# Kernel optimization log

Hardware: AMD Instinct MI355X
Metric: run time of the kernel (lower is better)

## Reference

```python
import math
import jax, jax.numpy as jnp
import numpy as np
from jax.scipy.linalg import solve_triangular

K, D, Q = 512, 2048, 8
B = 8192
EPS = 1e-5
RHO0 = math.log(math.exp(1.0) - 1.0)  # softplus^-1(1.0), matches psi_init=scale_init=1.0


def setup_inputs() -> dict:
    key = jax.random.key(0)
    k1, k2, k3, k4, k5 = jax.random.split(key, 5)
    x = jax.random.normal(k1, (B, D), dtype=jnp.float32)
    mu = jax.random.normal(k2, (K, D), dtype=jnp.float32)          # centroids
    dir_raw = jax.random.normal(k3, (K, D, Q), dtype=jnp.float32) / math.sqrt(D)
    scale_rho = jnp.full((K, Q), RHO0, dtype=jnp.float32) + 0.01 * jax.random.normal(k4, (K, Q), dtype=jnp.float32)
    psi_rho = jnp.full((D,), RHO0, dtype=jnp.float32) + 0.01 * jax.random.normal(k5, (D,), dtype=jnp.float32)
    pi_logits = jnp.zeros((K,), dtype=jnp.float32)
    return {"x": x, "mu": mu, "dir_raw": dir_raw, "scale_rho": scale_rho,
            "psi_rho": psi_rho, "pi_logits": pi_logits}


def _nll(x, mu, dir_raw, scale_rho, psi_rho, pi_logits):
    Dd = x.shape[1]
    q = dir_raw.shape[2]
    # diagonal noise (shared across components since psi_per_component=False)
    psi = jax.nn.softplus(psi_rho) + EPS                      # (D,)
    psi_inv = 1.0 / psi                                       # (D,)
    # factor loadings W_k = normalize(dir_raw, dim=1) * softplus(scale)
    n = jnp.maximum(jnp.linalg.norm(dir_raw, axis=1, keepdims=True), EPS)
    W = (dir_raw / n) * jax.nn.softplus(scale_rho)[:, None, :]  # (K, D, q)
    # Woodbury inner matrix M_k = I + W^T Psi^{-1} W and its Cholesky
    A = W * jnp.sqrt(psi_inv)[None, :, None]                  # (K, D, q)
    M = jnp.einsum('kdi,kdj->kij', A, A) + jnp.eye(q, dtype=W.dtype)[None]
    L = jnp.linalg.cholesky(M)                                # (K, q, q) lower
    # quadratic form pieces
    xT_Pinv_x = (x ** 2) @ psi_inv                            # (B,)
    xT_Pinv_mu = x @ (psi_inv[None, :] * mu).T                # (B, K)
    muT_Pinv_mu = jnp.sum(mu ** 2 * psi_inv[None, :], axis=-1)  # (K,)
    quad_Psi = xT_Pinv_x[:, None] - 2.0 * xT_Pinv_mu + muT_Pinv_mu[None, :]
    PinvW = psi_inv[None, :, None] * W                        # (K, D, q)
    WT_Pinv_x = jnp.einsum('bd,kdq->bkq', x, PinvW)           # (B, K, q)
    WT_Pinv_mu = jnp.einsum('kd,kdq->kq', mu, PinvW)          # (K, q)
    v = WT_Pinv_x - WT_Pinv_mu[None, :, :]                    # (B, K, q)
    # Ez = M^{-1} v via the Cholesky factor (batched over K, rhs over B)
    vT = jnp.transpose(v, (1, 2, 0))                          # (K, q, B)
    y = solve_triangular(L, vT, lower=True)
    EzT = solve_triangular(jnp.swapaxes(L, -1, -2), y, lower=False)
    Ez = jnp.transpose(EzT, (2, 0, 1))                        # (B, K, q)
    quad = quad_Psi - jnp.sum(v * Ez, axis=-1)                # (B, K)
    # log-determinants via Woodbury: log|C| = log|Psi| + log|M|
    logdet_Psi = jnp.sum(jnp.log(psi))                        # scalar (shared psi)
    logdet_M = 2.0 * jnp.sum(jnp.log(jnp.diagonal(L, axis1=-2, axis2=-1)), axis=-1)  # (K,)
    logdet_C = logdet_Psi + logdet_M                          # (K,)
    ll = -0.5 * (Dd * math.log(2.0 * math.pi) + logdet_C[None, :] + quad)  # (B, K)
    log_pi = jax.nn.log_softmax(pi_logits)
    logp = jax.scipy.special.logsumexp(ll + log_pi[None, :], axis=1)  # (B,)
    return jnp.mean(-logp)


def reference(x, mu, dir_raw, scale_rho, psi_rho, pi_logits):
    return _nll(x, mu, dir_raw, scale_rho, psi_rho, pi_logits)
```

## Files before the change

kernel.cpp:

```cpp
#include <hip/hip_runtime.h>

constexpr int Bn = 8192;
constexpr int Dd = 2048;
constexpr int Kk = 512;
constexpr int Qq = 8;
constexpr int Nn = Kk * 9;
constexpr float DLOG2PI = 3763.9722f;

constexpr int BM = 256, BN = 288, BK = 128;
constexpr int NT = Dd / BK;

constexpr float SX = 16.f;
constexpr float SW = 64.f;
constexpr float SG = 16.f;
constexpr float INV_UW = 1.f / (16.f * 64.f);
constexpr float INV_UG = 1.f / (16.f * 16.f);

constexpr size_t OFF_PSI   = 0;
constexpr size_t OFF_LDP   = 8192;
constexpr size_t OFF_LOGPI = 8448;
constexpr size_t OFF_OFFK  = 10752;
constexpr size_t OFF_MINV  = 13056;
constexpr size_t OFF_XPX   = 144384;
constexpr size_t OFF_XBF   = 177408;
constexpr size_t OFF_GT    = 33731840;
constexpr size_t OFF_LL    = 52606208;
constexpr size_t OFF_PART  = 69383424;

constexpr int LDS_AS   = 0;
constexpr int LDS_BS   = 65536;
constexpr int LDS_MINV = 139264;
constexpr int LDS_OFFC = 147584;
constexpr int LDS_TOT  = 147712;

typedef float f32x4 __attribute__((ext_vector_type(4)));
typedef int   i32x4v __attribute__((ext_vector_type(4)));
typedef int   i32x8v __attribute__((ext_vector_type(8)));
typedef __attribute__((address_space(3))) char lds_char;

__device__ inline float softplusf(float x) {
  return fmaxf(x, 0.f) + log1pf(expf(-fabsf(x)));
}
__device__ inline unsigned short f2bf(float x) {
  unsigned int u = __builtin_bit_cast(unsigned int, x);
  u = (u + 0x7fffu + ((u >> 16) & 1u)) >> 16;
  return (unsigned short)u;
}
__device__ inline unsigned int pack2(float a, float b) {
  return (unsigned int)f2bf(a) | ((unsigned int)f2bf(b) << 16);
}
__device__ inline float bf2f(unsigned int u16) {
  unsigned int v = u16 << 16;
  return __builtin_bit_cast(float, v);
}
__device__ inline unsigned char f2fp8(float x) {
  int v = __builtin_amdgcn_cvt_pk_fp8_f32(x, 0.f, 0, false);
  return (unsigned char)(v & 0xff);
}
__device__ inline void glds16(const unsigned char* g, char* l) {
  __builtin_amdgcn_global_load_lds(
      (const __attribute__((address_space(1))) unsigned int*)g,
      (__attribute__((address_space(3))) unsigned int*)l, 16, 0, 0);
}

#define BARRIER()                                   \
  do {                                              \
    asm volatile("" ::: "memory");                  \
    __builtin_amdgcn_s_barrier();                   \
    asm volatile("" ::: "memory");                  \
  } while (0)

#define DSR2(LO, HI, PL, PH, IMMS)                                    \
  asm volatile("ds_read_b128 %0, %2 offset:" IMMS "\n\t"              \
               "ds_read_b128 %1, %3 offset:" IMMS                     \
               : "=&v"(LO), "=&v"(HI)                                 \
               : "v"(PL), "v"(PH));

#define WAITLG(NS)                                                    \
  do {                                                                \
    asm volatile("s_waitcnt lgkmcnt(" NS ")" ::: "memory");           \
    __builtin_amdgcn_sched_barrier(0);                                \
  } while (0)

#define CAT8(D, LO, HI)                                               \
  do { D[0]=LO[0];D[1]=LO[1];D[2]=LO[2];D[3]=LO[3];                   \
       D[4]=HI[0];D[5]=HI[1];D[6]=HI[2];D[7]=HI[3]; } while (0)

__global__ __launch_bounds__(256) void prep_psi(
    const float* __restrict__ psi_rho, const float* __restrict__ pi_logits,
    float* __restrict__ psi_inv, float* __restrict__ logdetPsi,
    float* __restrict__ logpi) {
  __shared__ float red[256];
  int t = threadIdx.x;
  float acc = 0.f;
  for (int d = t; d < Dd; d += 256) {
    float p = softplusf(psi_rho[d]) + 1e-5f;
    psi_inv[d] = 1.f / p;
    acc += logf(p);
  }
  red[t] = acc;
  __syncthreads();
  for (int s = 128; s > 0; s >>= 1) { if (t < s) red[t] += red[t + s]; __syncthreads(); }
  if (t == 0) *logdetPsi = red[0];
  __syncthreads();
  float mx = -3.4e38f;
  for (int i = t; i < Kk; i += 256) mx = fmaxf(mx, pi_logits[i]);
  red[t] = mx;
  __syncthreads();
  for (int s = 128; s > 0; s >>= 1) { if (t < s) red[t] = fmaxf(red[t], red[t + s]); __syncthreads(); }
  mx = red[0];
  __syncthreads();
  float se = 0.f;
  for (int i = t; i < Kk; i += 256) se += expf(pi_logits[i] - mx);
  red[t] = se;
  __syncthreads();
  for (int s = 128; s > 0; s >>= 1) { if (t < s) red[t] += red[t + s]; __syncthreads(); }
  float lse = mx + logf(red[0]);
  for (int i = t; i < Kk; i += 256) logpi[i] = pi_logits[i] - lse;
}

#define TRI(i, j) ((i) * ((i) + 1) / 2 + (j))

__global__ __launch_bounds__(256) void prep_all(
    const float* __restrict__ x, const float* __restrict__ mu,
    const float* __restrict__ dir_raw, const float* __restrict__ scale_rho,
    const float* __restrict__ psi_inv,
    float* __restrict__ offk, float* __restrict__ Minv,
    unsigned char* __restrict__ Gq, unsigned char* __restrict__ xq,
    float* __restrict__ xPx) {
  __shared__ unsigned short sDir[Dd * 8];
  __shared__ float sPwmd[Dd];
  __shared__ float redk[4 * 53];
  __shared__ float R[53];
  __shared__ float sAl[8], sAh[8];
  __shared__ float sLt[36], sLdt[8];

  int bid = blockIdx.x;
  int t = threadIdx.x, lane = t & 63, w = t >> 6;

  if (bid >= Kk) {
    int b = bid - Kk;
    const float4* xr = (const float4*)(x + (size_t)b * Dd);
    const float4* pr = (const float4*)psi_inv;
    float4 v0 = xr[2 * t], v1 = xr[2 * t + 1];
    float4 p0 = pr[2 * t], p1 = pr[2 * t + 1];
    float acc = v0.x * v0.x * p0.x + v0.y * v0.y * p0.y + v0.z * v0.z * p0.z + v0.w * v0.w * p0.w
              + v1.x * v1.x * p1.x + v1.y * v1.y * p1.y + v1.z * v1.z * p1.z + v1.w * v1.w * p1.w;
    unsigned int q0 = (unsigned int)__builtin_amdgcn_cvt_pk_fp8_f32(SX * v0.x, SX * v0.y, 0, false);
    q0 = (unsigned int)__builtin_amdgcn_cvt_pk_fp8_f32(SX * v0.z, SX * v0.w, (int)q0, true);
    unsigned int q1 = (unsigned int)__builtin_amdgcn_cvt_pk_fp8_f32(SX * v1.x, SX * v1.y, 0, false);
    q1 = (unsigned int)__builtin_amdgcn_cvt_pk_fp8_f32(SX * v1.z, SX * v1.w, (int)q1, true);
    uint2 o; o.x = q0; o.y = q1;
    *(uint2*)(xq + (size_t)b * Dd + t * 8) = o;
#pragma unroll
    for (int s2 = 32; s2; s2 >>= 1) acc += __shfl_down(acc, s2, 64);
    float* r4 = sPwmd;
    if (lane == 0) r4[w] = acc;
    __syncthreads();
    if (t == 0) xPx[b] = r4[0] + r4[1] + r4[2] + r4[3];
    return;
  }

  int k = bid;
  float vals[53];
#pragma unroll
  for (int i = 0; i < 53; i++) vals[i] = 0.f;
  const float4* dirp = (const float4*)(dir_raw + (size_t)k * Dd * Qq);
  for (int d = t; d < Dd; d += 256) {
    float4 da = dirp[d * 2], db = dirp[d * 2 + 1];
    float dir8[8] = {da.x, da.y, da.z, da.w, db.x, db.y, db.z, db.w};
    float pw = psi_inv[d];
    float md = mu[(size_t)k * Dd + d];
    int c = 0;
#pragma unroll
    for (int i = 0; i < 8; i++) {
      float dip = dir8[i] * pw;
#pragma unroll
      for (int j = 0; j < 8; j++) {
        if (j < i) continue;
        vals[c] += dip * dir8[j]; c++;
      }
    }
#pragma unroll
    for (int q = 0; q < 8; q++) vals[36 + q] += dir8[q] * dir8[q];
    float mp = md * pw;
#pragma unroll
    for (int q = 0; q < 8; q++) vals[44 + q] += mp * dir8[q];
    vals[52] += md * mp;
    uint4 pk;
    pk.x = pack2(pw * dir8[0], pw * dir8[1]);
    pk.y = pack2(pw * dir8[2], pw * dir8[3]);
    pk.z = pack2(pw * dir8[4], pw * dir8[5]);
    pk.w = pack2(pw * dir8[6], pw * dir8[7]);
    *(uint4*)(sDir + d * 8) = pk;
    sPwmd[d] = mp;
  }
#pragma unroll
  for (int v = 0; v < 53; v++) {
    float val = vals[v];
#pragma unroll
    for (int o = 32; o; o >>= 1) val += __shfl_down(val, o, 64);
    if (lane == 0) redk[w * 53 + v] = val;
  }
  __syncthreads();
  if (t < 53) R[t] = redk[t] + redk[53 + t] + redk[106 + t] + redk[159 + t];
  __syncthreads();
  if (t == 0) {
    float Sf[8][8];
    {
      int c2 = 0;
#pragma unroll
      for (int i = 0; i < 8; i++) {
#pragma unroll
        for (int j = 0; j < 8; j++) {
          if (j < i) continue;
          float v = R[c2++]; Sf[i][j] = v; Sf[j][i] = v;
        }
      }
    }
    float alpha[8];
#pragma unroll
    for (int q = 0; q < 8; q++) {
      float nr = fmaxf(sqrtf(R[36 + q]), 1e-5f);
      alpha[q] = softplusf(scale_rho[(size_t)k * 8 + q]) / nr;
    }
    float Mm[8][8];
#pragma unroll
    for (int i = 0; i < 8; i++)
#pragma unroll
      for (int j = 0; j < 8; j++)
        Mm[i][j] = alpha[i] * alpha[j] * Sf[i][j] + (i == j ? 1.f : 0.f);
    float L[8][8], Ld[8];
#pragma unroll
    for (int i = 0; i < 8; i++) {
#pragma unroll
      for (int j = 0; j < 8; j++) {
        if (j > i) continue;
        float s2 = Mm[i][j];
#pragma unroll
        for (int p = 0; p < 8; p++) { if (p < j) s2 -= L[i][p] * L[j][p]; }
        if (i == j) { L[i][i] = sqrtf(s2); Ld[i] = 1.f / L[i][i]; }
        else        L[i][j] = s2 * Ld[j];
      }
    }
    float logdetM = 0.f;
#pragma unroll
    for (int i = 0; i < 8; i++) logdetM += 2.f * logf(L[i][i]);
    float wv[8];
#pragma unroll
    for (int q = 0; q < 8; q++) wv[q] = alpha[q] * R[44 + q];
    float y[8], h[8];
#pragma unroll
    for (int i = 0; i < 8; i++) {
      float s2 = wv[i];
#pragma unroll
      for (int p = 0; p < 8; p++) { if (p < i) s2 -= L[i][p] * y[p]; }
      y[i] = s2 * Ld[i];
    }
#pragma unroll
    for (int i = 7; i >= 0; i--) {
      float s2 = y[i];
#pragma unroll
      for (int p = 0; p < 8; p++) { if (p > i) s2 -= L[p][i] * h[p]; }
      h[i] = s2 * Ld[i];
    }
    float cc = R[52];
#pragma unroll
    for (int q = 0; q < 8; q++) cc -= wv[q] * h[q];
    {
      int c3 = 0;
#pragma unroll
      for (int i = 0; i < 8; i++)
#pragma unroll
        for (int j = 0; j < 8; j++) { if (j <= i) sLt[c3++] = L[i][j]; }
#pragma unroll
      for (int i = 0; i < 8; i++) sLdt[i] = Ld[i];
    }
    offk[k] = -0.5f * (DLOG2PI + logdetM + cc);
#pragma unroll
    for (int q = 0; q < 8; q++) { sAl[q] = alpha[q]; sAh[q] = alpha[q] * h[q]; }
  }
  __syncthreads();
  if (t < 8) {
    int col = t;
    float yy[8], z[8];
#pragma unroll
    for (int i = 0; i < 8; i++) {
      float s2 = (i == col) ? 1.f : 0.f;
#pragma unroll
      for (int p = 0; p < 8; p++) { if (p < i) s2 -= sLt[TRI(i, p)] * yy[p]; }
      yy[i] = s2 * sLdt[i];
    }
#pragma unroll
    for (int i = 7; i >= 0; i--) {
      float s2 = yy[i];
#pragma unroll
      for (int p = 0; p < 8; p++) { if (p > i) s2 -= sLt[TRI(p, i)] * z[p]; }
      z[i] = s2 * sLdt[i];
    }
#pragma unroll
    for (int r2 = 0; r2 < 8; r2++) Minv[(size_t)k * 64 + r2 * 8 + col] = z[r2];
  }
  float al[8], ah[8];
#pragma unroll
  for (int q = 0; q < 8; q++) { al[q] = sAl[q]; ah[q] = sAh[q]; }
  for (int d = t; d < Dd; d += 256) {
    uint4 pk = *(const uint4*)(sDir + d * 8);
    float pd[8];
    pd[0] = bf2f(pk.x & 0xffffu); pd[1] = bf2f(pk.x >> 16);
    pd[2] = bf2f(pk.y & 0xffffu); pd[3] = bf2f(pk.y >> 16);
    pd[4] = bf2f(pk.z & 0xffffu); pd[5] = bf2f(pk.z >> 16);
    pd[6] = bf2f(pk.w & 0xffffu); pd[7] = bf2f(pk.w >> 16);
    float gs = 0.f;
#pragma unroll
    for (int q = 0; q < 8; q++) {
      Gq[((size_t)(k * 9 + q)) * Dd + d] = f2fp8(SW * al[q] * pd[q]);
      gs += ah[q] * pd[q];
    }
    Gq[((size_t)(k * 9 + 8)) * Dd + d] = f2fp8(SG * (sPwmd[d] - gs));
  }
}

#define MFMA_COL(nt, bv)                                              \
  do {                                                                \
    acc[0][nt] = __builtin_amdgcn_mfma_scale_f32_16x16x128_f8f6f4(    \
        a0, bv, acc[0][nt], 0, 0, 0, 0x7f7f7f7f, 0, 0x7f7f7f7f);      \
    acc[1][nt] = __builtin_amdgcn_mfma_scale_f32_16x16x128_f8f6f4(    \
        a1, bv, acc[1][nt], 0, 0, 0, 0x7f7f7f7f, 0, 0x7f7f7f7f);      \
    acc[2][nt] = __builtin_amdgcn_mfma_scale_f32_16x16x128_f8f6f4(    \
        a2, bv, acc[2][nt], 0, 0, 0, 0x7f7f7f7f, 0, 0x7f7f7f7f);      \
    acc[3][nt] = __builtin_amdgcn_mfma_scale_f32_16x16x128_f8f6f4(    \
        a3, bv, acc[3][nt], 0, 0, 0, 0x7f7f7f7f, 0, 0x7f7f7f7f);      \
  } while (0)

__global__ __launch_bounds__(512, 1) void gemm_ll(
    const unsigned char* __restrict__ xq, const unsigned char* __restrict__ Gq,
    const float* __restrict__ Minv, const float* __restrict__ offk,
    const float* __restrict__ logpi, const float* __restrict__ logdetPsi,
    const float* __restrict__ xPx, float* __restrict__ ll) {
  __shared__ __align__(16) char smem[LDS_TOT];
  float* Cs    = (float*)smem;
  float* sMinv = (float*)(smem + LDS_MINV);
  float* sOff  = (float*)(smem + LDS_OFFC);
  lds_char* sm3 = (lds_char*)smem;

  int t = threadIdx.x, lane = t & 63, w = t >> 6;
  int wr = w >> 1, wc = w & 1;
  int m0 = blockIdx.y * BM;
  int n0 = blockIdx.x * BN;
  int comp0 = blockIdx.x * 32;

  for (int i = t; i < 2048; i += 512) {
    int cl = i >> 6, idx = i & 63;
    sMinv[cl * 65 + idx] = Minv[(size_t)comp0 * 64 + i];
  }
  if (t < 32)
    sOff[t] = offk[comp0 + t] + logpi[comp0 + t] - 0.5f * logdetPsi[0];

  f32x4 acc[4][9];
  f32x4 zero = {0.f, 0.f, 0.f, 0.f};
#pragma unroll
  for (int mt = 0; mt < 4; mt++)
#pragma unroll
    for (int nt = 0; nt < 9; nt++) acc[mt][nt] = zero;

  int rr  = lane >> 3;
  int cph = lane & 7;
  int csw = cph ^ rr;
  int quad = lane >> 4, r16 = lane & 15;
  int s8 = r16 & 7;
  int clo = (((2 * quad)     ^ s8) * 16);
  int chi = (((2 * quad + 1) ^ s8) * 16);
  const int aoff = (wr * 64 + r16) * 128;
  const int boff = (wc * 144 + r16) * 128;

  auto stage = [&](int buf, int k0) {
    if (w < 4) {
      char* dst = smem + LDS_AS + buf * 32768 + w * 8192;
      const unsigned char* src =
          xq + (size_t)(m0 + w * 64 + rr) * Dd + k0 + csw * 16;
#pragma unroll
      for (int i = 0; i < 8; ++i)
        glds16(src + (size_t)i * 8 * Dd, dst + i * 1024);
    } else {
      int w4 = w - 4;
      char* dst = smem + LDS_BS + buf * 36864 + w4 * 9216;
      const unsigned char* src =
          Gq + (size_t)(n0 + w4 * 72 + rr) * Dd + k0 + csw * 16;
#pragma unroll
      for (int i = 0; i < 9; ++i)
        glds16(src + (size_t)i * 8 * Dd, dst + i * 1024);
    }
  };

  stage(0, 0);
  asm volatile("s_waitcnt vmcnt(0) lgkmcnt(0)" ::: "memory");
  BARRIER();

#pragma unroll 1
  for (int tt = 0; tt < NT; ++tt) {
    int cur = tt & 1;
    lds_char* pAl = sm3 + (LDS_AS + cur * 32768) + aoff + clo;
    lds_char* pAh = sm3 + (LDS_AS + cur * 32768) + aoff + chi;
    lds_char* pBl = sm3 + (LDS_BS + cur * 36864) + boff + clo;
    lds_char* pBh = sm3 + (LDS_BS + cur * 36864) + boff + chi;
    if (tt < NT - 1) stage(cur ^ 1, (tt + 1) * BK);
    i32x4v a0l, a0h, a1l, a1h, a2l, a2h, a3l, a3h;
    i32x4v bXl, bXh, bYl, bYh, bZl, bZh;
    DSR2(a0l, a0h, pAl, pAh, "0")
    DSR2(a1l, a1h, pAl, pAh, "2048")
    DSR2(a2l, a2h, pAl, pAh, "4096")
    DSR2(a3l, a3h, pAl, pAh, "6144")
    DSR2(bXl, bXh, pBl, pBh, "0")
    DSR2(bYl, bYh, pBl, pBh, "2048")
    DSR2(bZl, bZh, pBl, pBh, "4096")
    i32x8v a0, a1, a2, a3, bq;
    WAITLG("4");
    CAT8(a0, a0l, a0h); CAT8(a1, a1l, a1h);
    CAT8(a2, a2l, a2h); CAT8(a3, a3l, a3h);
    CAT8(bq, bXl, bXh);
    MFMA_COL(0, bq);
    DSR2(bXl, bXh, pBl, pBh, "6144")
    WAITLG("4"); CAT8(bq, bYl, bYh); MFMA_COL(1, bq);
    DSR2(bYl, bYh, pBl, pBh, "8192")
    WAITLG("4"); CAT8(bq, bZl, bZh); MFMA_COL(2, bq);
    DSR2(bZl, bZh, pBl, pBh, "10240")
    WAITLG("4"); CAT8(bq, bXl, bXh); MFMA_COL(3, bq);
    DSR2(bXl, bXh, pBl, pBh, "12288")
    WAITLG("4"); CAT8(bq, bYl, bYh); MFMA_COL(4, bq);
    DSR2(bYl, bYh, pBl, pBh, "14336")
    WAITLG("4"); CAT8(bq, bZl, bZh); MFMA_COL(5, bq);
    DSR2(bZl, bZh, pBl, pBh, "16384")
    WAITLG("4"); CAT8(bq, bXl, bXh); MFMA_COL(6, bq);
    WAITLG("2"); CAT8(bq, bYl, bYh); MFMA_COL(7, bq);
    WAITLG("0"); CAT8(bq, bZl, bZh); MFMA_COL(8, bq);
    asm volatile("s_waitcnt vmcnt(0)" ::: "memory");
    BARRIER();
  }

  float P[36];
  {
    const float* Mi = sMinv + (wc * 16 + r16) * 65;
    int c = 0;
#pragma unroll
    for (int i2 = 0; i2 < 8; i2++) {
      P[c++] = 0.5f * Mi[i2 * 8 + i2];
#pragma unroll
      for (int j2 = i2 + 1; j2 < 8; j2++) P[c++] = Mi[i2 * 8 + j2];
    }
  }
  float offc = sOff[wc * 16 + r16];

  float* myC = Cs + w * (16 * 148);
#pragma unroll
  for (int mt = 0; mt < 4; ++mt) {
#pragma unroll
    for (int nt = 0; nt < 9; ++nt) {
#pragma unroll
      for (int r = 0; r < 4; r++) {
        myC[(quad * 4 + r) * 148 + nt * 16 + r16] = acc[mt][nt][r];
      }
    }
#pragma unroll
    for (int i = 0; i < 4; i++) {
      int row_l = quad + 4 * i;
      int b = m0 + wr * 64 + mt * 16 + row_l;
      const float* cp = myC + row_l * 148 + r16 * 9;
      float u[8];
#pragma unroll
      for (int j = 0; j < 8; j++) u[j] = cp[j] * INV_UW;
      float s = cp[8] * INV_UG;
      float tq = 0.f;
      int c = 0;
#pragma unroll
      for (int i2 = 0; i2 < 8; i2++) {
        float s2 = P[c++] * u[i2];
#pragma unroll
        for (int j2 = i2 + 1; j2 < 8; j2++) s2 += P[c++] * u[j2];
        tq += u[i2] * s2;
      }
      ll[(size_t)b * Kk + comp0 + wc * 16 + r16] = offc + s + tq - 0.5f * xPx[b];
    }
  }
}

__global__ __launch_bounds__(256) void lse_rows(
    const float* __restrict__ ll, float* __restrict__ part) {
  int t = threadIdx.x, lane = t & 63, w = t >> 6;
  int b = blockIdx.x * 4 + w;
  const float* row = ll + (size_t)b * Kk;
  float v[8];
  float mx = -3.4e38f;
#pragma unroll
  for (int i = 0; i < 8; i++) { v[i] = row[lane + 64 * i]; mx = fmaxf(mx, v[i]); }
#pragma unroll
  for (int o = 32; o; o >>= 1) mx = fmaxf(mx, __shfl_xor(mx, o, 64));
  float se = 0.f;
#pragma unroll
  for (int i = 0; i < 8; i++) se += expf(v[i] - mx);
#pragma unroll
  for (int o = 32; o; o >>= 1) se += __shfl_xor(se, o, 64);
  __shared__ float r4[4];
  if (lane == 0) r4[w] = -(mx + logf(se));
  __syncthreads();
  if (t == 0) part[blockIdx.x] = r4[0] + r4[1] + r4[2] + r4[3];
}

__global__ __launch_bounds__(256) void final_mean(
    const float* __restrict__ part, float* __restrict__ out) {
  int t = threadIdx.x, lane = t & 63, w = t >> 6;
  float acc = 0.f;
  for (int i = t; i < 2048; i += 256) acc += part[i];
#pragma unroll
  for (int o = 32; o; o >>= 1) acc += __shfl_down(acc, o, 64);
  __shared__ float r4[4];
  if (lane == 0) r4[w] = acc;
  __syncthreads();
  if (t == 0) out[0] = (r4[0] + r4[1] + r4[2] + r4[3]) * (1.0f / 8192.0f);
}

extern "C" void kernel_launch(void* const* d_in, const int* in_sizes, int n_in,
                              void* d_out, int out_size, void* d_ws, size_t ws_size,
                              hipStream_t stream) {
  const float* x         = (const float*)d_in[0];
  const float* mu        = (const float*)d_in[1];
  const float* dir_raw   = (const float*)d_in[2];
  const float* scale_rho = (const float*)d_in[3];
  const float* psi_rho   = (const float*)d_in[4];
  const float* pi_logits = (const float*)d_in[5];
  float* out = (float*)d_out;
  char* ws = (char*)d_ws;

  float* psi_inv          = (float*)(ws + OFF_PSI);
  float* logdetPsi        = (float*)(ws + OFF_LDP);
  float* logpi            = (float*)(ws + OFF_LOGPI);
  float* offk             = (float*)(ws + OFF_OFFK);
  float* Minv             = (float*)(ws + OFF_MINV);
  float* xPx              = (float*)(ws + OFF_XPX);
  unsigned char* xq       = (unsigned char*)(ws + OFF_XBF);
  unsigned char* Gq       = (unsigned char*)(ws + OFF_GT);
  float* ll               = (float*)(ws + OFF_LL);
  float* part             = (float*)(ws + OFF_PART);

  prep_psi<<<1, 256, 0, stream>>>(psi_rho, pi_logits, psi_inv, logdetPsi, logpi);
  prep_all<<<Kk + Bn, 256, 0, stream>>>(x, mu, dir_raw, scale_rho, psi_inv,
                                        offk, Minv, Gq, xq, xPx);
  dim3 g(Nn / BN, Bn / BM);
  gemm_ll<<<g, 512, 0, stream>>>(xq, Gq, Minv, offk, logpi, logdetPsi, xPx, ll);
  lse_rows<<<Bn / 4, 256, 0, stream>>>(ll, part);
  final_mean<<<1, 256, 0, stream>>>(part, out);
}
```

Before: 226.1 us.

## Pre-swizzle fp8 x into MFMA fragment layout and load A straight to registers

The x quantization kernel now writes fp8 x in a blocked layout that matches the per-lane MFMA A-fragment order. The GEMM loads each wave's A fragments directly from global memory into registers, one k-step ahead, instead of staging them through LDS. All eight waves now cooperate on staging the G tile into LDS, and the C scratch buffer gets its own LDS region. This aims to cut LDS traffic, staging work and LDS read latency in the main loop. The cost is duplicated global/L2 reads of A by the two waves sharing a row block, and correctness depends on the new vmcnt accounting for the in-flight register loads.

```diff
diff --git a/kernel.cpp b/kernel.cpp
--- a/kernel.cpp
+++ b/kernel.cpp
@@ -27,11 +27,11 @@
 constexpr size_t OFF_LL    = 52606208;
 constexpr size_t OFF_PART  = 69383424;
 
-constexpr int LDS_AS   = 0;
-constexpr int LDS_BS   = 65536;
-constexpr int LDS_MINV = 139264;
-constexpr int LDS_OFFC = 147584;
-constexpr int LDS_TOT  = 147712;
+constexpr int LDS_BS   = 0;
+constexpr int LDS_MINV = 73728;
+constexpr int LDS_OFFC = 82048;
+constexpr int LDS_CS   = 82176;
+constexpr int LDS_TOT  = 157952;
 
 typedef float f32x4 __attribute__((ext_vector_type(4)));
 typedef int   i32x4v __attribute__((ext_vector_type(4)));
@@ -151,7 +151,10 @@
     unsigned int q1 = (unsigned int)__builtin_amdgcn_cvt_pk_fp8_f32(SX * v1.x, SX * v1.y, 0, false);
     q1 = (unsigned int)__builtin_amdgcn_cvt_pk_fp8_f32(SX * v1.z, SX * v1.w, (int)q1, true);
     uint2 o; o.x = q0; o.y = q1;
-    *(uint2*)(xq + (size_t)b * Dd + t * 8) = o;
+    size_t dst = ((size_t)(b >> 4) * 16 + (size_t)(t >> 4)) * 2048
+               + (size_t)(((((t & 15) >> 2) << 4) | (b & 15))) * 32
+               + (size_t)(t & 3) * 8;
+    *(uint2*)(xq + dst) = o;
 #pragma unroll
     for (int s2 = 32; s2; s2 >>= 1) acc += __shfl_down(acc, s2, 64);
     float* r4 = sPwmd;
@@ -339,9 +342,9 @@
     const float* __restrict__ logpi, const float* __restrict__ logdetPsi,
     const float* __restrict__ xPx, float* __restrict__ ll) {
   __shared__ __align__(16) char smem[LDS_TOT];
-  float* Cs    = (float*)smem;
   float* sMinv = (float*)(smem + LDS_MINV);
   float* sOff  = (float*)(smem + LDS_OFFC);
+  float* Cs    = (float*)(smem + LDS_CS);
   lds_char* sm3 = (lds_char*)smem;
 
   int t = threadIdx.x, lane = t & 63, w = t >> 6;
@@ -371,28 +374,33 @@
   int s8 = r16 & 7;
   int clo = (((2 * quad)     ^ s8) * 16);
   int chi = (((2 * quad + 1) ^ s8) * 16);
-  const int aoff = (wr * 64 + r16) * 128;
   const int boff = (wc * 144 + r16) * 128;
+  const unsigned char* aP =
+      xq + ((size_t)(blockIdx.y * 16 + wr * 4)) * 32768 + (size_t)lane * 32;
 
   auto stage = [&](int buf, int k0) {
+    char* dst = smem + LDS_BS + buf * 36864;
     if (w < 4) {
-      char* dst = smem + LDS_AS + buf * 32768 + w * 8192;
-      const unsigned char* src =
-          xq + (size_t)(m0 + w * 64 + rr) * Dd + k0 + csw * 16;
-#pragma unroll
-      for (int i = 0; i < 8; ++i)
-        glds16(src + (size_t)i * 8 * Dd, dst + i * 1024);
+#pragma unroll
+      for (int i = 0; i < 5; ++i) {
+        int j = w * 5 + i;
+        glds16(Gq + (size_t)(n0 + j * 8 + rr) * Dd + k0 + csw * 16,
+               dst + j * 1024);
+      }
     } else {
-      int w4 = w - 4;
-      char* dst = smem + LDS_BS + buf * 36864 + w4 * 9216;
-      const unsigned char* src =
-          Gq + (size_t)(n0 + w4 * 72 + rr) * Dd + k0 + csw * 16;
-#pragma unroll
-      for (int i = 0; i < 9; ++i)
-        glds16(src + (size_t)i * 8 * Dd, dst + i * 1024);
+#pragma unroll
+      for (int i = 0; i < 4; ++i) {
+        int j = 20 + (w - 4) * 4 + i;
+        glds16(Gq + (size_t)(n0 + j * 8 + rr) * Dd + k0 + csw * 16,
+               dst + j * 1024);
+      }
     }
   };
 
+  i32x8v a0 = *(const i32x8v*)(aP);
+  i32x8v a1 = *(const i32x8v*)(aP + 32768);
+  i32x8v a2 = *(const i32x8v*)(aP + 65536);
+  i32x8v a3 = *(const i32x8v*)(aP + 98304);
   stage(0, 0);
   asm volatile("s_waitcnt vmcnt(0) lgkmcnt(0)" ::: "memory");
   BARRIER();
@@ -400,26 +408,15 @@
 #pragma unroll 1
   for (int tt = 0; tt < NT; ++tt) {
     int cur = tt & 1;
-    lds_char* pAl = sm3 + (LDS_AS + cur * 32768) + aoff + clo;
-    lds_char* pAh = sm3 + (LDS_AS + cur * 32768) + aoff + chi;
     lds_char* pBl = sm3 + (LDS_BS + cur * 36864) + boff + clo;
     lds_char* pBh = sm3 + (LDS_BS + cur * 36864) + boff + chi;
-    if (tt < NT - 1) stage(cur ^ 1, (tt + 1) * BK);
-    i32x4v a0l, a0h, a1l, a1h, a2l, a2h, a3l, a3h;
     i32x4v bXl, bXh, bYl, bYh, bZl, bZh;
-    DSR2(a0l, a0h, pAl, pAh, "0")
-    DSR2(a1l, a1h, pAl, pAh, "2048")
-    DSR2(a2l, a2h, pAl, pAh, "4096")
-    DSR2(a3l, a3h, pAl, pAh, "6144")
     DSR2(bXl, bXh, pBl, pBh, "0")
     DSR2(bYl, bYh, pBl, pBh, "2048")
     DSR2(bZl, bZh, pBl, pBh, "4096")
-    i32x8v a0, a1, a2, a3, bq;
-    WAITLG("4");
-    CAT8(a0, a0l, a0h); CAT8(a1, a1l, a1h);
-    CAT8(a2, a2l, a2h); CAT8(a3, a3l, a3h);
-    CAT8(bq, bXl, bXh);
-    MFMA_COL(0, bq);
+    if (tt < NT - 1) stage(cur ^ 1, (tt + 1) * BK);
+    i32x8v bq;
+    WAITLG("4"); CAT8(bq, bXl, bXh); MFMA_COL(0, bq);
     DSR2(bXl, bXh, pBl, pBh, "6144")
     WAITLG("4"); CAT8(bq, bYl, bYh); MFMA_COL(1, bq);
     DSR2(bYl, bYh, pBl, pBh, "8192")
@@ -434,7 +431,15 @@
     WAITLG("4"); CAT8(bq, bXl, bXh); MFMA_COL(6, bq);
     WAITLG("2"); CAT8(bq, bYl, bYh); MFMA_COL(7, bq);
     WAITLG("0"); CAT8(bq, bZl, bZh); MFMA_COL(8, bq);
-    asm volatile("s_waitcnt vmcnt(0)" ::: "memory");
+    __builtin_amdgcn_sched_barrier(0);
+    {
+      int kn = (tt + 1) & (NT - 1);
+      a0 = *(const i32x8v*)(aP +         (size_t)kn * 2048);
+      a1 = *(const i32x8v*)(aP + 32768 + (size_t)kn * 2048);
+      a2 = *(const i32x8v*)(aP + 65536 + (size_t)kn * 2048);
+      a3 = *(const i32x8v*)(aP + 98304 + (size_t)kn * 2048);
+    }
+    asm volatile("s_waitcnt vmcnt(8)" ::: "memory");
     BARRIER();
   }
 
```

New measurement: 233.1 us. 3.1% more time.
